# Performance work log

Measured on AMD Instinct MI355X. Metric: run time of the kernel, lower is better.

The kernel has to match this reference:

```python
import jax, jax.numpy as jnp
import numpy as np

N, S, W, H = 256, 64, 256, 32   # node_num, sensor_num, slide_win, gru_hid_size
ALPHA = 0.2
NEG = -9e15


def gat(h, adj, Wm, a):
    """pyGAT GraphAttentionLayer (concat=False, dropout=0 / eval).
    h: [..., M, din], adj: [..., M, M], Wm: [..., din, dout], a: [..., 2*dout]."""
    Wh = jnp.einsum('...mi,...io->...mo', h, Wm)
    dout = Wm.shape[-1]
    f1 = jnp.einsum('...mo,...o->...m', Wh, a[..., :dout])
    f2 = jnp.einsum('...mo,...o->...m', Wh, a[..., dout:])
    e = jax.nn.leaky_relu(f1[..., :, None] + f2[..., None, :], negative_slope=ALPHA)
    att = jax.nn.softmax(jnp.where(adj > 0, e, NEG), axis=-1)
    return jnp.einsum('...mk,...ko->...mo', att, Wh)


def gru_cell(h, x, Wih, Whh, bih, bhh):
    # per-node batched torch GRU cell; gate order r, z, n
    gi = jnp.einsum('ngi,ni->ng', Wih, x) + bih
    gh = jnp.einsum('ngh,nh->ng', Whh, h) + bhh
    ir, iz, inn = jnp.split(gi, 3, axis=-1)
    hr, hz, hn = jnp.split(gh, 3, axis=-1)
    r = jax.nn.sigmoid(ir + hr)
    z = jax.nn.sigmoid(iz + hz)
    n = jnp.tanh(inn + r * hn)
    return (1.0 - z) * n + z * h


def gru2(xseq, h0, Wih0, Whh0, bih0, bhh0, Wih1, Whh1, bih1, bhh1):
    # xseq: [N, S, Din] (seq axis = sensor axis), h0: [2, N, H] -> ([N,S,H], [2,N,H])
    def step(carry, x_t):
        h0c, h1c = carry
        h0n = gru_cell(h0c, x_t, Wih0, Whh0, bih0, bhh0)
        h1n = gru_cell(h1c, h0n, Wih1, Whh1, bih1, bhh1)
        return (h0n, h1n), h1n
    (h0f, h1f), ys = jax.lax.scan(step, (h0[0], h0[1]), jnp.swapaxes(xseq, 0, 1))
    return jnp.swapaxes(ys, 0, 1), jnp.stack([h0f, h1f])


def setup_inputs():
    key = jax.random.key(0)
    ks = jax.random.split(key, 32)
    def rn(k, shape, scale=0.05):
        return jax.random.normal(k, shape, dtype=jnp.float32) * scale
    inp = {}
    inp['x'] = jax.random.normal(ks[0], (N, S, W), dtype=jnp.float32)
    inp['Feature_adj_sub'] = jax.random.randint(ks[1], (N, S, S), 0, 2).astype(jnp.float32)
    inp['Time_adj_sub'] = jax.random.randint(ks[2], (N, W, W), 0, 2).astype(jnp.float32)
    inp['adj'] = jax.random.randint(ks[3], (N, N), 0, 2).astype(jnp.float32)
    inp['H_pre'] = jax.random.normal(ks[4], (2, N, H), dtype=jnp.float32)
    # per-node GAT params (stacked over nodes)
    inp['Fatt_W'] = rn(ks[5], (N, W, W)); inp['Fatt_a'] = rn(ks[6], (N, 2 * W))
    inp['Tatt_W'] = rn(ks[7], (N, S, S)); inp['Tatt_a'] = rn(ks[8], (N, 2 * S))
    # per-node 2-layer GRU params
    inp['Wih0'] = rn(ks[9], (N, 3 * H, 3 * W)); inp['Whh0'] = rn(ks[10], (N, 3 * H, H))
    inp['bih0'] = rn(ks[11], (N, 3 * H)); inp['bhh0'] = rn(ks[12], (N, 3 * H))
    inp['Wih1'] = rn(ks[13], (N, 3 * H, H)); inp['Whh1'] = rn(ks[14], (N, 3 * H, H))
    inp['bih1'] = rn(ks[15], (N, 3 * H)); inp['bhh1'] = rn(ks[16], (N, 3 * H))
    # per-node 3-layer FC
    inp['fc1_w'] = rn(ks[17], (N, H, H)); inp['fc1_b'] = rn(ks[18], (N, H))
    inp['fc2_w'] = rn(ks[19], (N, H, H)); inp['fc2_b'] = rn(ks[20], (N, H))
    inp['fc3_w'] = rn(ks[21], (N, 1, H)); inp['fc3_b'] = rn(ks[22], (N, 1))
    # global output GATs
    inp['oW'] = rn(ks[23], (S, S)); inp['oa'] = rn(ks[24], (2 * S,))
    inp['o1W'] = rn(ks[25], (S, S)); inp['o1a'] = rn(ks[26], (2 * S,))
    inp['o2W'] = rn(ks[27], (2 * S, S)); inp['o2a'] = rn(ks[28], (2 * S,))
    return inp


def reference(x, Feature_adj_sub, Time_adj_sub, adj, H_pre,
              Fatt_W, Fatt_a, Tatt_W, Tatt_a,
              Wih0, Whh0, bih0, bhh0, Wih1, Whh1, bih1, bhh1,
              fc1_w, fc1_b, fc2_w, fc2_b, fc3_w, fc3_b,
              oW, oa, o1W, o1a, o2W, o2a):
    # batched over all nodes at once (replaces Python loop over node_num)
    Fat = gat(x, Feature_adj_sub, Fatt_W, Fatt_a)                    # [N,S,W]
    Tat = gat(jnp.swapaxes(x, 1, 2), Time_adj_sub, Tatt_W, Tatt_a)   # [N,W,S]
    cat_at = jnp.concatenate([Fat, jnp.swapaxes(Tat, 1, 2), x], axis=-1)  # [N,S,3W]
    gru_out, cat_H = gru2(cat_at, H_pre, Wih0, Whh0, bih0, bhh0,
                          Wih1, Whh1, bih1, bhh1)                    # [N,S,H],[2,N,H]
    h = jax.nn.relu(jnp.einsum('nsh,nkh->nsk', gru_out, fc1_w) + fc1_b[:, None, :])
    h = jax.nn.relu(jnp.einsum('nsh,nkh->nsk', h, fc2_w) + fc2_b[:, None, :])
    ct = (jnp.einsum('nsh,nkh->nsk', h, fc3_w) + fc3_b[:, None, :])[..., 0]  # [N,S]
    out = gat(ct, adj, oW, oa)
    out1 = gat(ct, adj, o1W, o1a)
    finalout = gat(jnp.concatenate([out, out1], axis=-1), adj, o2W, o2a)
    return finalout, cat_H
```

## Files before the change

kernel.cpp:

```cpp
#include <hip/hip_runtime.h>
#include <hip/hip_bf16.h>

__device__ __forceinline__ float sigf(float x){ return __builtin_amdgcn_rcpf(1.f+__expf(-x)); }
__device__ __forceinline__ float tanhfa(float x){
  return 1.f - 2.f*__builtin_amdgcn_rcpf(1.f + __expf(2.f*x));
}

#define ALPHA 0.2f
#define NEGV  -9e15f


__device__ __forceinline__ void gl2lds16(const float* g, float* l){
  __builtin_amdgcn_global_load_lds(
      (const __attribute__((address_space(1))) void*)g,
      (__attribute__((address_space(3))) void*)l, 16, 0, 0);
}

__global__ __launch_bounds__(256) void k_mask(const float* __restrict__ src,
                                              unsigned* __restrict__ dst, int nelem){
  const int stride = gridDim.x * blockDim.x;
  const int lane = threadIdx.x & 63;
  for (int e = blockIdx.x*blockDim.x + threadIdx.x; e < nelem; e += stride){
    unsigned long long m = __ballot(src[e] > 0.f);
    if (lane == 0)       dst[e >> 5] = (unsigned)m;
    else if (lane == 32) dst[e >> 5] = (unsigned)(m >> 32);
  }
}

__global__ __launch_bounds__(256) void k3_wht(const float* __restrict__ x,
                                              const float* __restrict__ TW,
                                              const float* __restrict__ Ta,
                                              float* __restrict__ WhTt,
                                              float* __restrict__ Tf1p,
                                              float* __restrict__ Tf2p){
  const int n = blockIdx.x >> 1, ch = blockIdx.x & 1, c0 = ch*32;
  const int tid = threadIdx.x;
  __shared__ float Wm[64][36];
  __shared__ float as1[32], as2[32];
  for (int idx = tid; idx < 2048; idx += 256){
    int k = idx >> 5, cc = idx & 31;
    Wm[k][cc] = TW[n*4096 + k*64 + c0 + cc];
  }
  if (tid < 32){ as1[tid] = Ta[n*128 + c0 + tid]; as2[tid] = Ta[n*128 + 64 + c0 + tid]; }
  __syncthreads();
  const int i = tid;
  const float* xn = x + n*16384;
  float acc[32];
#pragma unroll
  for (int c = 0; c < 32; ++c) acc[c] = 0.f;
#pragma unroll 2
  for (int k = 0; k < 64; ++k){
    float xv = xn[k*256 + i];
    const float* wr = &Wm[k][0];
#pragma unroll
    for (int c = 0; c < 32; ++c) acc[c] = fmaf(xv, wr[c], acc[c]);
  }
  float f1 = 0.f, f2 = 0.f;
#pragma unroll
  for (int c = 0; c < 32; ++c){ f1 = fmaf(acc[c], as1[c], f1); f2 = fmaf(acc[c], as2[c], f2); }
  Tf1p[ch*65536 + n*256 + i] = f1;
  Tf2p[ch*65536 + n*256 + i] = f2;
  float* o = WhTt + n*16384 + i*64 + c0;
#pragma unroll
  for (int q = 0; q < 8; ++q)
    *(float4*)&o[4*q] = make_float4(acc[4*q], acc[4*q+1], acc[4*q+2], acc[4*q+3]);
}

__global__ __launch_bounds__(256) void k4_tat(const float* __restrict__ WhTt,
                                              const float* __restrict__ Tf1p,
                                              const float* __restrict__ Tf2p,
                                              const unsigned* __restrict__ maskT,
                                              float* __restrict__ TatT){
  const int n = blockIdx.x >> 1, ch = blockIdx.x & 1, c0 = ch*32;
  const int tid = threadIdx.x;
  __shared__ float wtL[8192];
  __shared__ float ptb[8192];
  __shared__ float f2s[256];
  __shared__ float ssum[256];
  __shared__ float wmax[4];
  {
    const int w = tid >> 6, l = tid & 63;
    const float* src = WhTt + n*16384 + (w*64 + (l>>3))*64 + c0 + (l&7)*4;
    float* dst = &wtL[w*2048];
#pragma unroll
    for (int r = 0; r < 8; ++r) gl2lds16(src + r*512, dst + r*256);
  }
  const float f1  = Tf1p[n*256 + tid] + Tf1p[65536 + n*256 + tid];
  const float f2v = Tf2p[n*256 + tid] + Tf2p[65536 + n*256 + tid];
  f2s[tid] = f2v;
  unsigned mw[8];
#pragma unroll
  for (int w = 0; w < 8; ++w) mw[w] = maskT[n*2048 + tid*8 + w];
  float wm = f2v;
#pragma unroll
  for (int d = 1; d < 64; d <<= 1) wm = fmaxf(wm, __shfl_xor(wm, d));
  if ((tid & 63) == 0) wmax[tid >> 6] = wm;
  asm volatile("s_waitcnt vmcnt(0)" ::: "memory");
  __syncthreads();
  const float mb = fmaxf(fmaxf(wmax[0], wmax[1]), fmaxf(wmax[2], wmax[3]));
  const float tm = f1 + mb;
  const float m  = (tm > 0.f) ? tm : ALPHA*tm;
  const int iq = tid & 63, cq = tid >> 6;
  float acc[4][8];
#pragma unroll
  for (int r = 0; r < 4; ++r)
#pragma unroll
    for (int c = 0; c < 8; ++c) acc[r][c] = 0.f;
  float sloc = 0.f;
  for (int jt = 0; jt < 8; ++jt){
    const int j0 = jt*32;
#pragma unroll
    for (int jj = 0; jj < 32; jj += 4){
      const float4 f2q = *(const float4*)&f2s[j0 + jj];
      const unsigned mk = mw[(j0 + jj) >> 5];
      const int sh = (j0 + jj) & 31;
      float t0 = f1 + f2q.x; t0 = (t0 > 0.f) ? t0 : ALPHA*t0;
      float t1 = f1 + f2q.y; t1 = (t1 > 0.f) ? t1 : ALPHA*t1;
      float t2 = f1 + f2q.z; t2 = (t2 > 0.f) ? t2 : ALPHA*t2;
      float t3 = f1 + f2q.w; t3 = (t3 > 0.f) ? t3 : ALPHA*t3;
      const float e0 = ((mk >> (sh+0)) & 1u) ? __expf(t0 - m) : 0.f;
      const float e1 = ((mk >> (sh+1)) & 1u) ? __expf(t1 - m) : 0.f;
      const float e2 = ((mk >> (sh+2)) & 1u) ? __expf(t2 - m) : 0.f;
      const float e3 = ((mk >> (sh+3)) & 1u) ? __expf(t3 - m) : 0.f;
      sloc += (e0 + e1) + (e2 + e3);
      ptb[(jj+0)*256 + tid] = e0;
      ptb[(jj+1)*256 + tid] = e1;
      ptb[(jj+2)*256 + tid] = e2;
      ptb[(jj+3)*256 + tid] = e3;
    }
    __syncthreads();
#pragma unroll 4
    for (int jj = 0; jj < 32; ++jj){
      const float4 p4 = *(const float4*)&ptb[jj*256 + 4*iq];
      const float4 w0 = *(const float4*)&wtL[(j0+jj)*32 + cq*8];
      const float4 w1 = *(const float4*)&wtL[(j0+jj)*32 + cq*8 + 4];
#pragma unroll
      for (int r = 0; r < 4; ++r){
        const float pv = (r == 0) ? p4.x : (r == 1) ? p4.y : (r == 2) ? p4.z : p4.w;
        acc[r][0] = fmaf(pv, w0.x, acc[r][0]);
        acc[r][1] = fmaf(pv, w0.y, acc[r][1]);
        acc[r][2] = fmaf(pv, w0.z, acc[r][2]);
        acc[r][3] = fmaf(pv, w0.w, acc[r][3]);
        acc[r][4] = fmaf(pv, w1.x, acc[r][4]);
        acc[r][5] = fmaf(pv, w1.y, acc[r][5]);
        acc[r][6] = fmaf(pv, w1.z, acc[r][6]);
        acc[r][7] = fmaf(pv, w1.w, acc[r][7]);
      }
    }
    __syncthreads();
  }
  ssum[tid] = sloc;
  __syncthreads();
  float* o = TatT + n*16384;
#pragma unroll
  for (int r = 0; r < 4; ++r){
    const int i2 = 4*iq + r;
    const float sv = ssum[i2];
    const float inv = (sv > 0.f) ? __builtin_amdgcn_rcpf(sv) : 0.f;
#pragma unroll
    for (int cc = 0; cc < 8; ++cc)
      o[(c0 + cq*8 + cc)*256 + i2] = acc[r][cc] * inv;
  }
}

__global__ __launch_bounds__(256) void k1_whf(const float* __restrict__ x,
                                              const float* __restrict__ FW,
                                              float* __restrict__ WhF){
  const int n = blockIdx.x >> 1, ch = blockIdx.x & 1, c0 = ch*128;
  const int tid = threadIdx.x;
  __shared__ float xt[16384];
  {
    const int w = tid >> 6, l = tid & 63;
    const float* xg = x + n*16384 + w*4096 + l*4;
    float* ld = &xt[w*4096];
#pragma unroll
    for (int j = 0; j < 16; ++j) gl2lds16(xg + j*256, ld + j*256);
  }
  asm volatile("s_waitcnt vmcnt(0)" ::: "memory");
  __syncthreads();
  const int cq = tid & 31, iq = tid >> 5;
  const int cc = c0 + cq*4;
  const float* Wn = FW + (size_t)n*65536 + cc;
  const float* xrow = &xt[iq*8*256];
  float acc[8][4];
#pragma unroll
  for (int i = 0; i < 8; ++i)
#pragma unroll
    for (int c = 0; c < 4; ++c) acc[i][c] = 0.f;
#pragma unroll 2
  for (int k4 = 0; k4 < 64; ++k4){
    const float4 w0 = *(const float4*)&Wn[(4*k4+0)*256];
    const float4 w1 = *(const float4*)&Wn[(4*k4+1)*256];
    const float4 w2 = *(const float4*)&Wn[(4*k4+2)*256];
    const float4 w3 = *(const float4*)&Wn[(4*k4+3)*256];
#pragma unroll
    for (int i = 0; i < 8; ++i){
      const float4 xv = *(const float4*)&xrow[i*256 + 4*k4];
      acc[i][0] = fmaf(xv.x, w0.x, acc[i][0]); acc[i][0] = fmaf(xv.y, w1.x, acc[i][0]);
      acc[i][0] = fmaf(xv.z, w2.x, acc[i][0]); acc[i][0] = fmaf(xv.w, w3.x, acc[i][0]);
      acc[i][1] = fmaf(xv.x, w0.y, acc[i][1]); acc[i][1] = fmaf(xv.y, w1.y, acc[i][1]);
      acc[i][1] = fmaf(xv.z, w2.y, acc[i][1]); acc[i][1] = fmaf(xv.w, w3.y, acc[i][1]);
      acc[i][2] = fmaf(xv.x, w0.z, acc[i][2]); acc[i][2] = fmaf(xv.y, w1.z, acc[i][2]);
      acc[i][2] = fmaf(xv.z, w2.z, acc[i][2]); acc[i][2] = fmaf(xv.w, w3.z, acc[i][2]);
      acc[i][3] = fmaf(xv.x, w0.w, acc[i][3]); acc[i][3] = fmaf(xv.y, w1.w, acc[i][3]);
      acc[i][3] = fmaf(xv.z, w2.w, acc[i][3]); acc[i][3] = fmaf(xv.w, w3.w, acc[i][3]);
    }
  }
  float* o = WhF + n*16384 + cc;
#pragma unroll
  for (int i = 0; i < 8; ++i)
    *(float4*)&o[(iq*8 + i)*256] = make_float4(acc[i][0], acc[i][1], acc[i][2], acc[i][3]);
}

__global__ __launch_bounds__(512) void k2_fat(const float* __restrict__ WhF,
                                              const float* __restrict__ Fa,
                                              const float* __restrict__ Fadj,
                                              float* __restrict__ Fat){
  const int n = blockIdx.x, tid = threadIdx.x;
  __shared__ float attT[64][68];
  __shared__ float f1s[64], f2s[64];
  __shared__ float part[64][8][2];
  const float* Wh = WhF + n*16384;
  {
    int i = tid >> 3, q = tid & 7;
    const float* an = Fa + n*512;
    float p1 = 0.f, p2 = 0.f;
    for (int cc = 0; cc < 32; ++cc){
      int c2 = q*32 + cc;
      float w = Wh[i*256 + c2];
      p1 = fmaf(w, an[c2], p1);
      p2 = fmaf(w, an[256 + c2], p2);
    }
    part[i][q][0] = p1; part[i][q][1] = p2;
  }
  __syncthreads();
  if (tid < 64){
    float s1 = 0.f, s2 = 0.f;
#pragma unroll
    for (int q = 0; q < 8; ++q){ s1 += part[tid][q][0]; s2 += part[tid][q][1]; }
    f1s[tid] = s1; f2s[tid] = s2;
  }
  __syncthreads();
  if (tid < 64){
    const int r = tid;
    const float f1 = f1s[r];
    const float* adjr = Fadj + n*4096 + r*64;
    unsigned m0 = 0, m1 = 0;
#pragma unroll
    for (int j = 0; j < 32; ++j) if (adjr[j] > 0.f) m0 |= (1u << j);
#pragma unroll
    for (int j = 0; j < 32; ++j) if (adjr[32+j] > 0.f) m1 |= (1u << j);
    float m = -INFINITY;
#pragma unroll
    for (int j = 0; j < 64; ++j){
      float e = f1 + f2s[j]; e = (e > 0.f) ? e : ALPHA*e;
      unsigned bit = (j < 32) ? ((m0 >> j) & 1u) : ((m1 >> (j-32)) & 1u);
      e = bit ? e : NEGV;
      m = fmaxf(m, e);
    }
    float s = 0.f;
#pragma unroll
    for (int j = 0; j < 64; ++j){
      float e = f1 + f2s[j]; e = (e > 0.f) ? e : ALPHA*e;
      unsigned bit = (j < 32) ? ((m0 >> j) & 1u) : ((m1 >> (j-32)) & 1u);
      e = bit ? e : NEGV;
      s += __expf(e - m);
    }
    const float inv = 1.f / s;
#pragma unroll
    for (int j = 0; j < 64; ++j){
      float e = f1 + f2s[j]; e = (e > 0.f) ? e : ALPHA*e;
      unsigned bit = (j < 32) ? ((m0 >> j) & 1u) : ((m1 >> (j-32)) & 1u);
      e = bit ? e : NEGV;
      attT[j][r] = __expf(e - m) * inv;
    }
  }
  __syncthreads();
  const int c = tid & 255, ih = tid >> 8;
  float acc[32];
#pragma unroll
  for (int i = 0; i < 32; ++i) acc[i] = 0.f;
#pragma unroll 2
  for (int j = 0; j < 64; ++j){
    float w = Wh[j*256 + c];
    const float* ar = &attT[j][ih*32];
#pragma unroll
    for (int i = 0; i < 32; ++i) acc[i] = fmaf(ar[i], w, acc[i]);
  }
  float* o = Fat + n*16384;
#pragma unroll
  for (int i = 0; i < 32; ++i) o[(ih*32 + i)*256 + c] = acc[i];
}

__global__ __launch_bounds__(256) void k5_gi0(const float* __restrict__ Fat,
                                              const float* __restrict__ TatT,
                                              const float* __restrict__ x,
                                              const float* __restrict__ Wih0,
                                              float* __restrict__ P0,
                                              float* __restrict__ P1,
                                              float* __restrict__ P2){
  const int n = blockIdx.x & 255, s = blockIdx.x >> 8;
  const int tid = threadIdx.x;
  const int l = tid & 63, w = tid >> 6;
  const int a = tid & 31, b = tid >> 5;
  __shared__ float cl[2][2048];
  __shared__ float wl[2][3072];
  const float* src = (s == 0) ? (Fat + n*16384)
                   : (s == 1) ? (TatT + n*16384)
                              : (x + n*16384);
  const float* Wseg = Wih0 + (size_t)n*73728 + s*256;
  const int lr = l >> 3, lc = l & 7, sc = lc ^ lr;
  const float* cg0 = src + (16*w + lr)*256 + sc*4;
  const float* cg1 = cg0 + 8*256;
  const float* wg0 = Wseg + (size_t)(24*w + lr)*768 + lc*4;
  const float* wg1 = wg0 + (size_t)8*768;
  const float* wg2 = wg0 + (size_t)16*768;

#define K5_STAGE(BF, K0) do {                       \
    gl2lds16(cg0 + (K0), &cl[BF][512*w]);           \
    gl2lds16(cg1 + (K0), &cl[BF][512*w + 256]);     \
    gl2lds16(wg0 + (K0), &wl[BF][768*w]);           \
    gl2lds16(wg1 + (K0), &wl[BF][768*w + 256]);     \
    gl2lds16(wg2 + (K0), &wl[BF][768*w + 512]);     \
  } while (0)

  float acc[12][2];
#pragma unroll
  for (int gi = 0; gi < 12; ++gi){ acc[gi][0] = 0.f; acc[gi][1] = 0.f; }

  int bf = 0;
  K5_STAGE(0, 0);
  const int ax4 = (a & 7) << 2;
#pragma unroll 1
  for (int kt = 0; kt < 8; ++kt){
    if (kt < 7){
      K5_STAGE(bf ^ 1, (kt + 1) * 32);
      asm volatile("s_waitcnt vmcnt(5)" ::: "memory");
    } else {
      asm volatile("s_waitcnt vmcnt(0)" ::: "memory");
    }
    __builtin_amdgcn_s_barrier();
    const float* clb  = &cl[bf][a*32];
    const float* clb2 = &cl[bf][(a+32)*32];
    const float* wlb  = &wl[bf][b*384];
#pragma unroll
    for (int k4 = 0; k4 < 8; ++k4){
      const int j4 = (k4 << 2) ^ ax4;
      const float4 c0 = *(const float4*)&clb[j4];
      const float4 c1 = *(const float4*)&clb2[j4];
#pragma unroll
      for (int gi = 0; gi < 12; ++gi){
        const float4 wv = *(const float4*)&wlb[gi*32 + (k4 << 2)];
        float a0 = acc[gi][0], a1 = acc[gi][1];
        a0 = fmaf(wv.x, c0.x, a0); a1 = fmaf(wv.x, c1.x, a1);
        a0 = fmaf(wv.y, c0.y, a0); a1 = fmaf(wv.y, c1.y, a1);
        a0 = fmaf(wv.z, c0.z, a0); a1 = fmaf(wv.z, c1.z, a1);
        a0 = fmaf(wv.w, c0.w, a0); a1 = fmaf(wv.w, c1.w, a1);
        acc[gi][0] = a0; acc[gi][1] = a1;
      }
    }
    __builtin_amdgcn_s_barrier();
    bf ^= 1;
  }
#undef K5_STAGE
  float* o = (s == 0) ? (P0 + n*16384)
           : (s == 1) ? (P1 + n*16384)
                      : (P2 + n*8192);
#pragma unroll
  for (int q = 0; q < 3; ++q){
    *(float4*)&o[a*96 + b*12 + q*4] =
        make_float4(acc[4*q][0], acc[4*q+1][0], acc[4*q+2][0], acc[4*q+3][0]);
    *(float4*)&o[(a+32)*96 + b*12 + q*4] =
        make_float4(acc[4*q][1], acc[4*q+1][1], acc[4*q+2][1], acc[4*q+3][1]);
  }
}

__global__ __launch_bounds__(128) void k6_gru(const float* __restrict__ G0,
                                              const float* __restrict__ G1,
                                              const float* __restrict__ G2,
                                              const float* __restrict__ Hpre,
                                              const float* __restrict__ Whh0,
                                              const float* __restrict__ bih0,
                                              const float* __restrict__ bhh0,
                                              const float* __restrict__ Wih1,
                                              const float* __restrict__ Whh1,
                                              const float* __restrict__ bih1,
                                              const float* __restrict__ bhh1,
                                              const float* __restrict__ fc1w,
                                              const float* __restrict__ fc1b,
                                              const float* __restrict__ fc2w,
                                              const float* __restrict__ fc2b,
                                              const float* __restrict__ fc3w,
                                              const float* __restrict__ fc3b,
                                              float* __restrict__ ct,
                                              float* __restrict__ dout){
  const int n = blockIdx.x, tid = threadIdx.x;
  const int wid = tid >> 6, l = tid & 63;
  const int g2 = l & 31, co = (l >> 5) * 16;
  __shared__ float ginS[6144];
  __shared__ float h0buf[2][32];
  __shared__ float h1buf[2][32];
  __shared__ float hist[64][33];
  __shared__ float Wst[32][33];
  __shared__ float b1s[32], b2s[32], w3s[32];
  {
    const float4* p0 = (const float4*)(G0 + n*16384);
    const float4* p1 = (const float4*)(G1 + n*16384);
    const float4* p2 = (const float4*)(G2 + n*8192);
    float4* gs = (float4*)ginS;
#pragma unroll
    for (int j = 0; j < 12; ++j){
      int idx = j*128 + tid;
      float4 a = p0[idx], b = p1[idx], c = p2[idx];
      gs[idx] = make_float4(a.x+b.x+c.x, a.y+b.y+c.y, a.z+b.z+c.z, a.w+b.w+c.w);
    }
  }
  if (tid < 32){
    b1s[tid] = fc1b[n*32 + tid];
    b2s[tid] = fc2b[n*32 + tid];
    w3s[tid] = fc3w[n*32 + tid];
  }
  for (int idx = tid; idx < 1024; idx += 128) Wst[idx>>5][idx&31] = fc1w[n*1024 + idx];
  float wr_[16], wz_[16], wn_[16];
  float ur_[16], uz_[16], un_[16];
  {
    const float* WA = (wid == 0) ? (Whh0 + n*3072) : (Wih1 + n*3072);
#pragma unroll
    for (int q = 0; q < 4; ++q){
      float4 v;
      v = *(const float4*)(WA + g2*32 + co + 4*q);       wr_[4*q]=v.x; wr_[4*q+1]=v.y; wr_[4*q+2]=v.z; wr_[4*q+3]=v.w;
      v = *(const float4*)(WA + (32+g2)*32 + co + 4*q);  wz_[4*q]=v.x; wz_[4*q+1]=v.y; wz_[4*q+2]=v.z; wz_[4*q+3]=v.w;
      v = *(const float4*)(WA + (64+g2)*32 + co + 4*q);  wn_[4*q]=v.x; wn_[4*q+1]=v.y; wn_[4*q+2]=v.z; wn_[4*q+3]=v.w;
    }
    if (wid == 1){
      const float* WB = Whh1 + n*3072;
#pragma unroll
      for (int q = 0; q < 4; ++q){
        float4 v;
        v = *(const float4*)(WB + g2*32 + co + 4*q);       ur_[4*q]=v.x; ur_[4*q+1]=v.y; ur_[4*q+2]=v.z; ur_[4*q+3]=v.w;
        v = *(const float4*)(WB + (32+g2)*32 + co + 4*q);  uz_[4*q]=v.x; uz_[4*q+1]=v.y; uz_[4*q+2]=v.z; uz_[4*q+3]=v.w;
        v = *(const float4*)(WB + (64+g2)*32 + co + 4*q);  un_[4*q]=v.x; un_[4*q+1]=v.y; un_[4*q+2]=v.z; un_[4*q+3]=v.w;
      }
    }
  }
  const float* bip = (wid == 0) ? bih0 : bih1;
  const float* bhp = (wid == 0) ? bhh0 : bhh1;
  const float br = bip[n*96 + g2], bz = bip[n*96 + 32 + g2], bn = bip[n*96 + 64 + g2];
  const float cr = bhp[n*96 + g2], cz = bhp[n*96 + 32 + g2], cn = bhp[n*96 + 64 + g2];
  const float* hp = (wid == 0) ? (Hpre + n*32) : (Hpre + 8192 + n*32);
  float hown = hp[g2];
  float hs[16];
#pragma unroll
  for (int q = 0; q < 4; ++q){
    float4 v = *(const float4*)&hp[co + 4*q];
    hs[4*q]=v.x; hs[4*q+1]=v.y; hs[4*q+2]=v.z; hs[4*q+3]=v.w;
  }
  for (int s = 0; s < 65; ++s){
    __syncthreads();
    if (wid == 0){
      if (s < 64){
        const float gr = ginS[s*96 + g2], gz = ginS[s*96 + 32 + g2], gn = ginS[s*96 + 64 + g2];
        if (s > 0){
#pragma unroll
          for (int q = 0; q < 4; ++q){
            float4 v = *(const float4*)&h0buf[(s-1)&1][co + 4*q];
            hs[4*q]=v.x; hs[4*q+1]=v.y; hs[4*q+2]=v.z; hs[4*q+3]=v.w;
          }
        }
        float pr = 0.f, pz = 0.f, pn = 0.f;
#pragma unroll
        for (int j = 0; j < 16; ++j){
          pr = fmaf(wr_[j], hs[j], pr);
          pz = fmaf(wz_[j], hs[j], pz);
          pn = fmaf(wn_[j], hs[j], pn);
        }
        pr += __shfl_xor(pr, 32);
        pz += __shfl_xor(pz, 32);
        pn += __shfl_xor(pn, 32);
        const float r = sigf(gr + br + pr + cr);
        const float z = sigf(gz + bz + pz + cz);
        const float nn = tanhfa(gn + bn + r*(pn + cn));
        hown = (1.f - z)*nn + z*hown;
        if (l < 32) h0buf[s & 1][g2] = hown;
      }
    } else {
      if (s >= 1){
        const int t = s - 1;
        if (s > 1){
#pragma unroll
          for (int q = 0; q < 4; ++q){
            float4 v = *(const float4*)&h1buf[(s-1)&1][co + 4*q];
            hs[4*q]=v.x; hs[4*q+1]=v.y; hs[4*q+2]=v.z; hs[4*q+3]=v.w;
          }
        }
        float hx[16];
#pragma unroll
        for (int q = 0; q < 4; ++q){
          float4 v = *(const float4*)&h0buf[(s-1)&1][co + 4*q];
          hx[4*q]=v.x; hx[4*q+1]=v.y; hx[4*q+2]=v.z; hx[4*q+3]=v.w;
        }
        float qr = 0.f, qz = 0.f, qn = 0.f, sr = 0.f, sz = 0.f, sn = 0.f;
#pragma unroll
        for (int j = 0; j < 16; ++j){
          qr = fmaf(wr_[j], hx[j], qr);  sr = fmaf(ur_[j], hs[j], sr);
          qz = fmaf(wz_[j], hx[j], qz);  sz = fmaf(uz_[j], hs[j], sz);
          qn = fmaf(wn_[j], hx[j], qn);  sn = fmaf(un_[j], hs[j], sn);
        }
        float vr = qr + sr; vr += __shfl_xor(vr, 32);
        float vz = qz + sz; vz += __shfl_xor(vz, 32);
        qn += __shfl_xor(qn, 32);
        sn += __shfl_xor(sn, 32);
        const float r1 = sigf(vr + br + cr);
        const float z1 = sigf(vz + bz + cz);
        const float n1 = tanhfa(qn + bn + r1*(sn + cn));
        hown = (1.f - z1)*n1 + z1*hown;
        if (l < 32){ h1buf[s & 1][g2] = hown; hist[t][g2] = hown; }
      }
    }
  }
  if (wid == 0 && l < 32) dout[16384 + n*32 + g2] = hown;
  if (wid == 1 && l < 32) dout[16384 + 8192 + n*32 + g2] = hown;
  __syncthreads();
  float r1a[32];
  if (tid < 64){
    float hr[32];
#pragma unroll
    for (int k = 0; k < 32; ++k) hr[k] = hist[tid][k];
#pragma unroll
    for (int k = 0; k < 32; ++k){
      float a0=0.f,a1=0.f,a2=0.f,a3=0.f;
#pragma unroll
      for (int q = 0; q < 32; q += 4){
        a0 = fmaf(hr[q],   Wst[k][q],   a0);
        a1 = fmaf(hr[q+1], Wst[k][q+1], a1);
        a2 = fmaf(hr[q+2], Wst[k][q+2], a2);
        a3 = fmaf(hr[q+3], Wst[k][q+3], a3);
      }
      float v = b1s[k] + ((a0+a1)+(a2+a3));
      r1a[k] = v > 0.f ? v : 0.f;
    }
  }
  __syncthreads();
  for (int idx = tid; idx < 1024; idx += 128) Wst[idx>>5][idx&31] = fc2w[n*1024 + idx];
  __syncthreads();
  if (tid < 64){
    float r2a[32];
#pragma unroll
    for (int k = 0; k < 32; ++k){
      float a0=0.f,a1=0.f,a2=0.f,a3=0.f;
#pragma unroll
      for (int q = 0; q < 32; q += 4){
        a0 = fmaf(r1a[q],   Wst[k][q],   a0);
        a1 = fmaf(r1a[q+1], Wst[k][q+1], a1);
        a2 = fmaf(r1a[q+2], Wst[k][q+2], a2);
        a3 = fmaf(r1a[q+3], Wst[k][q+3], a3);
      }
      float v = b2s[k] + ((a0+a1)+(a2+a3));
      r2a[k] = v > 0.f ? v : 0.f;
    }
    float v = fc3b[n];
#pragma unroll
    for (int k = 0; k < 32; ++k) v = fmaf(r2a[k], w3s[k], v);
    ct[n*64 + tid] = v;
  }
}

__global__ __launch_bounds__(256) void k8a(const float* __restrict__ ct,
                                           const float* __restrict__ W0,
                                           const float* __restrict__ a0,
                                           const float* __restrict__ W1,
                                           const float* __restrict__ a1,
                                           float* __restrict__ WhABt,
                                           float* __restrict__ OF1,
                                           float* __restrict__ OF2){
  const int gat = blockIdx.x >> 2, rq = blockIdx.x & 3, r0 = rq*64;
  const int tid = threadIdx.x;
  const int ii = tid & 63, cq = tid >> 6;
  __shared__ float ctl[64][65];
  __shared__ float Wl[64][68];
  __shared__ float a1s[64], a2s[64];
  __shared__ float red[64][4][2];
  const float* W = gat ? W1 : W0;
  const float* aa = gat ? a1 : a0;
  for (int idx = tid; idx < 4096; idx += 256){
    int i2 = idx >> 6, k = idx & 63;
    ctl[i2][k] = ct[(r0 + i2)*64 + k];
  }
  for (int idx = tid; idx < 4096; idx += 256){
    int k = idx >> 6, c = idx & 63;
    Wl[k][c] = W[k*64 + c];
  }
  if (tid < 64){ a1s[tid] = aa[tid]; a2s[tid] = aa[64 + tid]; }
  __syncthreads();
  float acc[16];
#pragma unroll
  for (int c = 0; c < 16; ++c) acc[c] = 0.f;
#pragma unroll 2
  for (int k = 0; k < 64; ++k){
    float v = ctl[ii][k];
    const float* wr = &Wl[k][cq*16];
#pragma unroll
    for (int c = 0; c < 16; ++c) acc[c] = fmaf(v, wr[c], acc[c]);
  }
  float p1 = 0.f, p2 = 0.f;
#pragma unroll
  for (int c = 0; c < 16; ++c){
    p1 = fmaf(acc[c], a1s[cq*16 + c], p1);
    p2 = fmaf(acc[c], a2s[cq*16 + c], p2);
  }
  red[ii][cq][0] = p1; red[ii][cq][1] = p2;
  float* o = WhABt + gat*16384;
#pragma unroll
  for (int c = 0; c < 16; ++c) o[(cq*16 + c)*256 + r0 + ii] = acc[c];
  __syncthreads();
  if (cq == 0){
    OF1[gat*256 + r0 + ii] = red[ii][0][0] + red[ii][1][0] + red[ii][2][0] + red[ii][3][0];
    OF2[gat*256 + r0 + ii] = red[ii][0][1] + red[ii][1][1] + red[ii][2][1] + red[ii][3][1];
  }
}

__global__ __launch_bounds__(256) void k8b(const float* __restrict__ WhABt,
                                           const float* __restrict__ OF1,
                                           const float* __restrict__ OF2,
                                           const unsigned* __restrict__ maskA,
                                           float* __restrict__ OUTT){
  const int gat = blockIdx.x >> 2, c0 = (blockIdx.x & 3) * 16;
  const int i = threadIdx.x;
  __shared__ float wt[4096];
  __shared__ float f2s[256];
  __shared__ float wmax[4];
  {
    const int w = i >> 6, l = i & 63;
    const float* src = WhABt + gat*16384 + c0*256 + w*1024 + l*4;
    float* dst = &wt[w*1024];
#pragma unroll
    for (int r = 0; r < 4; ++r) gl2lds16(src + r*256, dst + r*256);
  }
  const float f1  = OF1[gat*256 + i];
  const float f2v = OF2[gat*256 + i];
  f2s[i] = f2v;
  unsigned mw[8];
#pragma unroll
  for (int w = 0; w < 8; ++w) mw[w] = maskA[i*8 + w];
  float wm = f2v;
#pragma unroll
  for (int d = 1; d < 64; d <<= 1) wm = fmaxf(wm, __shfl_xor(wm, d));
  if ((i & 63) == 0) wmax[i >> 6] = wm;
  asm volatile("s_waitcnt vmcnt(0)" ::: "memory");
  __syncthreads();
  const float mb = fmaxf(fmaxf(wmax[0], wmax[1]), fmaxf(wmax[2], wmax[3]));
  const float tm = f1 + mb;
  const float m  = (tm > 0.f) ? tm : ALPHA*tm;
  float acc[16];
#pragma unroll
  for (int c = 0; c < 16; ++c) acc[c] = 0.f;
  float s = 0.f;
#pragma unroll 2
  for (int jb = 0; jb < 64; ++jb){
    const float4 f2q = *(const float4*)&f2s[jb*4];
    const unsigned mk = mw[jb >> 3];
    const int sh = (jb & 7) * 4;
    float t0 = f1 + f2q.x; t0 = (t0 > 0.f) ? t0 : ALPHA*t0;
    float t1 = f1 + f2q.y; t1 = (t1 > 0.f) ? t1 : ALPHA*t1;
    float t2 = f1 + f2q.z; t2 = (t2 > 0.f) ? t2 : ALPHA*t2;
    float t3 = f1 + f2q.w; t3 = (t3 > 0.f) ? t3 : ALPHA*t3;
    const float e0 = ((mk >> (sh+0)) & 1u) ? __expf(t0 - m) : 0.f;
    const float e1 = ((mk >> (sh+1)) & 1u) ? __expf(t1 - m) : 0.f;
    const float e2 = ((mk >> (sh+2)) & 1u) ? __expf(t2 - m) : 0.f;
    const float e3 = ((mk >> (sh+3)) & 1u) ? __expf(t3 - m) : 0.f;
    s += (e0 + e1) + (e2 + e3);
#pragma unroll
    for (int c = 0; c < 16; ++c){
      const float4 wv = *(const float4*)&wt[c*256 + jb*4];
      acc[c] = fmaf(e0, wv.x, fmaf(e1, wv.y, fmaf(e2, wv.z, fmaf(e3, wv.w, acc[c]))));
    }
  }
  const float inv = (s > 0.f) ? __builtin_amdgcn_rcpf(s) : 0.f;
#pragma unroll
  for (int c = 0; c < 16; ++c) OUTT[gat*16384 + (c0+c)*256 + i] = acc[c] * inv;
}

__global__ __launch_bounds__(256) void k8c(const float* __restrict__ OUTT,
                                           const float* __restrict__ W2,
                                           const float* __restrict__ a2,
                                           float* __restrict__ Wh2,
                                           float* __restrict__ F1B,
                                           float* __restrict__ F2B){
  const int r0 = blockIdx.x * 32;
  const int tid = threadIdx.x;
  const int ii = tid & 31, cq = tid >> 5;
  __shared__ float W2l[128][68];
  __shared__ float a1s[64], a2s[64];
  __shared__ float red[32][8][2];
  for (int idx = tid; idx < 8192; idx += 256){
    int k = idx >> 6, c = idx & 63;
    W2l[k][c] = W2[k*64 + c];
  }
  if (tid < 64){ a1s[tid] = a2[tid]; a2s[tid] = a2[64 + tid]; }
  __syncthreads();
  float acc[8];
#pragma unroll
  for (int c = 0; c < 8; ++c) acc[c] = 0.f;
#pragma unroll 2
  for (int k = 0; k < 128; ++k){
    float v = OUTT[(k >> 6)*16384 + (k & 63)*256 + r0 + ii];
    const float* wr = &W2l[k][cq*8];
#pragma unroll
    for (int c = 0; c < 8; ++c) acc[c] = fmaf(v, wr[c], acc[c]);
  }
  float p1 = 0.f, p2 = 0.f;
#pragma unroll
  for (int c = 0; c < 8; ++c){
    p1 = fmaf(acc[c], a1s[cq*8 + c], p1);
    p2 = fmaf(acc[c], a2s[cq*8 + c], p2);
  }
  red[ii][cq][0] = p1; red[ii][cq][1] = p2;
#pragma unroll
  for (int c = 0; c < 8; ++c) Wh2[(cq*8 + c)*256 + r0 + ii] = acc[c];
  __syncthreads();
  if (cq == 0){
    float s1 = 0.f, s2 = 0.f;
#pragma unroll
    for (int q = 0; q < 8; ++q){ s1 += red[ii][q][0]; s2 += red[ii][q][1]; }
    F1B[r0 + ii] = s1; F2B[r0 + ii] = s2;
  }
}

__global__ __launch_bounds__(256) void k8d(const float* __restrict__ Wh2,
                                           const float* __restrict__ F1B,
                                           const float* __restrict__ F2B,
                                           const unsigned* __restrict__ maskA,
                                           float* __restrict__ dOut){
  const int c0 = blockIdx.x * 16;
  const int i = threadIdx.x;
  __shared__ float wt[4096];
  __shared__ float f2s[256];
  __shared__ float wmax[4];
  {
    const int w = i >> 6, l = i & 63;
    const float* src = Wh2 + c0*256 + w*1024 + l*4;
    float* dst = &wt[w*1024];
#pragma unroll
    for (int r = 0; r < 4; ++r) gl2lds16(src + r*256, dst + r*256);
  }
  const float f1  = F1B[i];
  const float f2v = F2B[i];
  f2s[i] = f2v;
  unsigned mw[8];
#pragma unroll
  for (int w = 0; w < 8; ++w) mw[w] = maskA[i*8 + w];
  float wm = f2v;
#pragma unroll
  for (int d = 1; d < 64; d <<= 1) wm = fmaxf(wm, __shfl_xor(wm, d));
  if ((i & 63) == 0) wmax[i >> 6] = wm;
  asm volatile("s_waitcnt vmcnt(0)" ::: "memory");
  __syncthreads();
  const float mb = fmaxf(fmaxf(wmax[0], wmax[1]), fmaxf(wmax[2], wmax[3]));
  const float tm = f1 + mb;
  const float m  = (tm > 0.f) ? tm : ALPHA*tm;
  float acc[16];
#pragma unroll
  for (int c = 0; c < 16; ++c) acc[c] = 0.f;
  float s = 0.f;
#pragma unroll 2
  for (int jb = 0; jb < 64; ++jb){
    const float4 f2q = *(const float4*)&f2s[jb*4];
    const unsigned mk = mw[jb >> 3];
    const int sh = (jb & 7) * 4;
    float t0 = f1 + f2q.x; t0 = (t0 > 0.f) ? t0 : ALPHA*t0;
    float t1 = f1 + f2q.y; t1 = (t1 > 0.f) ? t1 : ALPHA*t1;
    float t2 = f1 + f2q.z; t2 = (t2 > 0.f) ? t2 : ALPHA*t2;
    float t3 = f1 + f2q.w; t3 = (t3 > 0.f) ? t3 : ALPHA*t3;
    const float e0 = ((mk >> (sh+0)) & 1u) ? __expf(t0 - m) : 0.f;
    const float e1 = ((mk >> (sh+1)) & 1u) ? __expf(t1 - m) : 0.f;
    const float e2 = ((mk >> (sh+2)) & 1u) ? __expf(t2 - m) : 0.f;
    const float e3 = ((mk >> (sh+3)) & 1u) ? __expf(t3 - m) : 0.f;
    s += (e0 + e1) + (e2 + e3);
#pragma unroll
    for (int c = 0; c < 16; ++c){
      const float4 wv = *(const float4*)&wt[c*256 + jb*4];
      acc[c] = fmaf(e0, wv.x, fmaf(e1, wv.y, fmaf(e2, wv.z, fmaf(e3, wv.w, acc[c]))));
    }
  }
  const float inv = (s > 0.f) ? __builtin_amdgcn_rcpf(s) : 0.f;
#pragma unroll
  for (int c = 0; c < 16; ++c) dOut[i*64 + c0 + c] = acc[c] * inv;
}

extern "C" void kernel_launch(void* const* d_in, const int* in_sizes, int n_in,
                              void* d_out, int out_size, void* d_ws, size_t ws_size,
                              hipStream_t stream){
  (void)in_sizes; (void)n_in; (void)out_size; (void)ws_size;
  const float* x     = (const float*)d_in[0];
  const float* Fadj  = (const float*)d_in[1];
  const float* Tadj  = (const float*)d_in[2];
  const float* adj   = (const float*)d_in[3];
  const float* Hpre  = (const float*)d_in[4];
  const float* FattW = (const float*)d_in[5];
  const float* Fatta = (const float*)d_in[6];
  const float* TattW = (const float*)d_in[7];
  const float* Tatta = (const float*)d_in[8];
  const float* Wih0  = (const float*)d_in[9];
  const float* Whh0  = (const float*)d_in[10];
  const float* bih0  = (const float*)d_in[11];
  const float* bhh0  = (const float*)d_in[12];
  const float* Wih1  = (const float*)d_in[13];
  const float* Whh1  = (const float*)d_in[14];
  const float* bih1  = (const float*)d_in[15];
  const float* bhh1  = (const float*)d_in[16];
  const float* fc1w  = (const float*)d_in[17];
  const float* fc1b  = (const float*)d_in[18];
  const float* fc2w  = (const float*)d_in[19];
  const float* fc2b  = (const float*)d_in[20];
  const float* fc3w  = (const float*)d_in[21];
  const float* fc3b  = (const float*)d_in[22];
  const float* oW    = (const float*)d_in[23];
  const float* oa    = (const float*)d_in[24];
  const float* o1W   = (const float*)d_in[25];
  const float* o1a   = (const float*)d_in[26];
  const float* o2W   = (const float*)d_in[27];
  const float* o2a   = (const float*)d_in[28];
  float* out = (float*)d_out;

  float* ws = (float*)d_ws;
  float* R0 = ws;
  float* R1 = ws + 4194304;
  float* R2 = ws + 8388608;
  unsigned* maskT = (unsigned*)R2;
  float* Tf1p = R2 + 524288;
  float* Tf2p = R2 + 655360;
  unsigned* maskA = (unsigned*)(ws + 12582912);
  float* WhTt = R0;
  float* WhF  = R0;
  float* TatT = R1;
  float* Fat  = R2;
  float* P0 = R2;
  float* P1 = R1;
  float* P2 = R0;
  float* ctb   = R0 + 2097152;
  float* WhABt = R1 + 16384;
  float* OF1   = R1 + 49152;
  float* OF2   = R1 + 49664;
  float* OUTT  = R1 + 50176;
  float* WH2   = R1 + 82944;
  float* F1B   = R1 + 99328;
  float* F2B   = R1 + 99584;

  k_mask<<<1024, 256, 0, stream>>>(Tadj, maskT, 16777216);
  k_mask<<<32, 256, 0, stream>>>(adj, maskA, 65536);
  k3_wht<<<512, 256, 0, stream>>>(x, TattW, Tatta, WhTt, Tf1p, Tf2p);
  k4_tat<<<512, 256, 0, stream>>>(WhTt, Tf1p, Tf2p, maskT, TatT);
  k1_whf<<<512, 256, 0, stream>>>(x, FattW, WhF);
  k2_fat<<<256, 512, 0, stream>>>(WhF, Fatta, Fadj, Fat);
  k5_gi0<<<768, 256, 0, stream>>>(Fat, TatT, x, Wih0, P0, P1, P2);
  k6_gru<<<256, 128, 0, stream>>>(P0, P1, P2, Hpre, Whh0, bih0, bhh0, Wih1, Whh1, bih1, bhh1,
                                  fc1w, fc1b, fc2w, fc2b, fc3w, fc3b, ctb, out);
  k8a<<<8, 256, 0, stream>>>(ctb, oW, oa, o1W, o1a, WhABt, OF1, OF2);
  k8b<<<8, 256, 0, stream>>>(WhABt, OF1, OF2, maskA, OUTT);
  k8c<<<8, 256, 0, stream>>>(OUTT, o2W, o2a, WH2, F1B, F2B);
  k8d<<<4, 256, 0, stream>>>(WH2, F1B, F2B, maskA, out);
}
```

Measured before the change: 605.2 us.

## Read GRU input weights directly from global memory; stage activations via registers

```diff
diff --git a/kernel.cpp b/kernel.cpp
--- a/kernel.cpp
+++ b/kernel.cpp
@@ -301,68 +301,60 @@
                                               float* __restrict__ P2){
   const int n = blockIdx.x & 255, s = blockIdx.x >> 8;
   const int tid = threadIdx.x;
-  const int l = tid & 63, w = tid >> 6;
   const int a = tid & 31, b = tid >> 5;
-  __shared__ float cl[2][2048];
-  __shared__ float wl[2][3072];
+  __shared__ float cl[2][2304];
   const float* src = (s == 0) ? (Fat + n*16384)
                    : (s == 1) ? (TatT + n*16384)
                               : (x + n*16384);
-  const float* Wseg = Wih0 + (size_t)n*73728 + s*256;
-  const int lr = l >> 3, lc = l & 7, sc = lc ^ lr;
-  const float* cg0 = src + (16*w + lr)*256 + sc*4;
-  const float* cg1 = cg0 + 8*256;
-  const float* wg0 = Wseg + (size_t)(24*w + lr)*768 + lc*4;
-  const float* wg1 = wg0 + (size_t)8*768;
-  const float* wg2 = wg0 + (size_t)16*768;
-
-#define K5_STAGE(BF, K0) do {                       \
-    gl2lds16(cg0 + (K0), &cl[BF][512*w]);           \
-    gl2lds16(cg1 + (K0), &cl[BF][512*w + 256]);     \
-    gl2lds16(wg0 + (K0), &wl[BF][768*w]);           \
-    gl2lds16(wg1 + (K0), &wl[BF][768*w + 256]);     \
-    gl2lds16(wg2 + (K0), &wl[BF][768*w + 512]);     \
-  } while (0)
-
+  const float* Wseg = Wih0 + (size_t)n*73728 + s*256 + (size_t)b*12*768;
+  const int tr = tid >> 2, kq = tid & 3;
+  const float* cg = src + tr*256 + kq*8;
+  const int cwo = tr*36 + kq*8;
+  {
+    float4 ra = *(const float4*)cg;
+    float4 rb = *(const float4*)(cg + 4);
+    *(float4*)&cl[0][cwo]     = ra;
+    *(float4*)&cl[0][cwo + 4] = rb;
+  }
+  __syncthreads();
   float acc[12][2];
 #pragma unroll
   for (int gi = 0; gi < 12; ++gi){ acc[gi][0] = 0.f; acc[gi][1] = 0.f; }
-
-  int bf = 0;
-  K5_STAGE(0, 0);
-  const int ax4 = (a & 7) << 2;
 #pragma unroll 1
   for (int kt = 0; kt < 8; ++kt){
+    const int buf = kt & 1;
+    float4 na, nb;
     if (kt < 7){
-      K5_STAGE(bf ^ 1, (kt + 1) * 32);
-      asm volatile("s_waitcnt vmcnt(5)" ::: "memory");
-    } else {
-      asm volatile("s_waitcnt vmcnt(0)" ::: "memory");
-    }
-    __builtin_amdgcn_s_barrier();
-    const float* clb  = &cl[bf][a*32];
-    const float* clb2 = &cl[bf][(a+32)*32];
-    const float* wlb  = &wl[bf][b*384];
+      na = *(const float4*)(cg + (kt+1)*32);
+      nb = *(const float4*)(cg + (kt+1)*32 + 4);
+    }
+    const float* Wk = Wseg + kt*32;
+    const float* c0p = &cl[buf][a*36];
+    const float* c1p = &cl[buf][(a+32)*36];
 #pragma unroll
     for (int k4 = 0; k4 < 8; ++k4){
-      const int j4 = (k4 << 2) ^ ax4;
-      const float4 c0 = *(const float4*)&clb[j4];
-      const float4 c1 = *(const float4*)&clb2[j4];
+      float4 wv[12];
+#pragma unroll
+      for (int gi = 0; gi < 12; ++gi)
+        wv[gi] = *(const float4*)(Wk + (size_t)gi*768 + k4*4);
+      const float4 c0 = *(const float4*)(c0p + k4*4);
+      const float4 c1 = *(const float4*)(c1p + k4*4);
 #pragma unroll
       for (int gi = 0; gi < 12; ++gi){
-        const float4 wv = *(const float4*)&wlb[gi*32 + (k4 << 2)];
         float a0 = acc[gi][0], a1 = acc[gi][1];
-        a0 = fmaf(wv.x, c0.x, a0); a1 = fmaf(wv.x, c1.x, a1);
-        a0 = fmaf(wv.y, c0.y, a0); a1 = fmaf(wv.y, c1.y, a1);
-        a0 = fmaf(wv.z, c0.z, a0); a1 = fmaf(wv.z, c1.z, a1);
-        a0 = fmaf(wv.w, c0.w, a0); a1 = fmaf(wv.w, c1.w, a1);
+        a0 = fmaf(wv[gi].x, c0.x, a0); a1 = fmaf(wv[gi].x, c1.x, a1);
+        a0 = fmaf(wv[gi].y, c0.y, a0); a1 = fmaf(wv[gi].y, c1.y, a1);
+        a0 = fmaf(wv[gi].z, c0.z, a0); a1 = fmaf(wv[gi].z, c1.z, a1);
+        a0 = fmaf(wv[gi].w, c0.w, a0); a1 = fmaf(wv[gi].w, c1.w, a1);
         acc[gi][0] = a0; acc[gi][1] = a1;
       }
     }
-    __builtin_amdgcn_s_barrier();
-    bf ^= 1;
-  }
-#undef K5_STAGE
+    if (kt < 7){
+      *(float4*)&cl[buf^1][cwo]     = na;
+      *(float4*)&cl[buf^1][cwo + 4] = nb;
+    }
+    __syncthreads();
+  }
   float* o = (s == 0) ? (P0 + n*16384)
            : (s == 1) ? (P1 + n*16384)
                       : (P2 + n*8192);
```

New measurement: 655.7 us. 1.08x slower.

## Retile GRU input-projection kernel to 4 rows per thread with split-K reduction

Applied to the files above, without the earlier changes.

```diff
diff --git a/kernel.cpp b/kernel.cpp
--- a/kernel.cpp
+++ b/kernel.cpp
@@ -302,16 +302,20 @@
   const int n = blockIdx.x & 255, s = blockIdx.x >> 8;
   const int tid = threadIdx.x;
   const int l = tid & 63, w = tid >> 6;
-  const int a = tid & 31, b = tid >> 5;
+  const int b = tid >> 5;
+  const int kg = (tid >> 4) & 1;
+  const int ta = tid & 15;
   __shared__ float cl[2][2048];
   __shared__ float wl[2][3072];
   const float* src = (s == 0) ? (Fat + n*16384)
                    : (s == 1) ? (TatT + n*16384)
                               : (x + n*16384);
   const float* Wseg = Wih0 + (size_t)n*73728 + s*256;
-  const int lr = l >> 3, lc = l & 7, sc = lc ^ lr;
-  const float* cg0 = src + (16*w + lr)*256 + sc*4;
-  const float* cg1 = cg0 + 8*256;
+  const int lr = l >> 3, lc = l & 7;
+  const int sc0 = lc ^ ((4*w + (lr >> 2)) & 7);
+  const int sc1 = lc ^ ((4*w + 2 + (lr >> 2)) & 7);
+  const float* cg0 = src + (16*w + lr)*256 + sc0*4;
+  const float* cg1 = src + (16*w + 8 + lr)*256 + sc1*4;
   const float* wg0 = Wseg + (size_t)(24*w + lr)*768 + lc*4;
   const float* wg1 = wg0 + (size_t)8*768;
   const float* wg2 = wg0 + (size_t)16*768;
@@ -324,13 +328,15 @@
     gl2lds16(wg2 + (K0), &wl[BF][768*w + 512]);     \
   } while (0)
 
-  float acc[12][2];
-#pragma unroll
-  for (int gi = 0; gi < 12; ++gi){ acc[gi][0] = 0.f; acc[gi][1] = 0.f; }
+  float acc[12][4];
+#pragma unroll
+  for (int gi = 0; gi < 12; ++gi)
+#pragma unroll
+    for (int r = 0; r < 4; ++r) acc[gi][r] = 0.f;
 
   int bf = 0;
   K5_STAGE(0, 0);
-  const int ax4 = (a & 7) << 2;
+  const int t7 = ta & 7;
 #pragma unroll 1
   for (int kt = 0; kt < 8; ++kt){
     if (kt < 7){
@@ -340,38 +346,60 @@
       asm volatile("s_waitcnt vmcnt(0)" ::: "memory");
     }
     __builtin_amdgcn_s_barrier();
-    const float* clb  = &cl[bf][a*32];
-    const float* clb2 = &cl[bf][(a+32)*32];
-    const float* wlb  = &wl[bf][b*384];
-#pragma unroll
-    for (int k4 = 0; k4 < 8; ++k4){
-      const int j4 = (k4 << 2) ^ ax4;
-      const float4 c0 = *(const float4*)&clb[j4];
-      const float4 c1 = *(const float4*)&clb2[j4];
+    const float* wb = &wl[bf][b*384 + kg*16];
+    const float* cb = &cl[bf][ta*128];
+#pragma unroll
+    for (int k4 = 0; k4 < 4; ++k4){
+      const int q4 = (((kg*4 + k4) ^ t7)) * 4;
+      const float4 c0 = *(const float4*)&cb[0*32 + q4];
+      const float4 c1 = *(const float4*)&cb[1*32 + q4];
+      const float4 c2 = *(const float4*)&cb[2*32 + q4];
+      const float4 c3 = *(const float4*)&cb[3*32 + q4];
 #pragma unroll
       for (int gi = 0; gi < 12; ++gi){
-        const float4 wv = *(const float4*)&wlb[gi*32 + (k4 << 2)];
-        float a0 = acc[gi][0], a1 = acc[gi][1];
+        const float4 wv = *(const float4*)&wb[gi*32 + k4*4];
+        float a0 = acc[gi][0], a1 = acc[gi][1], a2 = acc[gi][2], a3 = acc[gi][3];
         a0 = fmaf(wv.x, c0.x, a0); a1 = fmaf(wv.x, c1.x, a1);
+        a2 = fmaf(wv.x, c2.x, a2); a3 = fmaf(wv.x, c3.x, a3);
         a0 = fmaf(wv.y, c0.y, a0); a1 = fmaf(wv.y, c1.y, a1);
+        a2 = fmaf(wv.y, c2.y, a2); a3 = fmaf(wv.y, c3.y, a3);
         a0 = fmaf(wv.z, c0.z, a0); a1 = fmaf(wv.z, c1.z, a1);
+        a2 = fmaf(wv.z, c2.z, a2); a3 = fmaf(wv.z, c3.z, a3);
         a0 = fmaf(wv.w, c0.w, a0); a1 = fmaf(wv.w, c1.w, a1);
-        acc[gi][0] = a0; acc[gi][1] = a1;
+        a2 = fmaf(wv.w, c2.w, a2); a3 = fmaf(wv.w, c3.w, a3);
+        acc[gi][0] = a0; acc[gi][1] = a1; acc[gi][2] = a2; acc[gi][3] = a3;
       }
     }
     __builtin_amdgcn_s_barrier();
     bf ^= 1;
   }
 #undef K5_STAGE
-  float* o = (s == 0) ? (P0 + n*16384)
-           : (s == 1) ? (P1 + n*16384)
-                      : (P2 + n*8192);
-#pragma unroll
-  for (int q = 0; q < 3; ++q){
-    *(float4*)&o[a*96 + b*12 + q*4] =
-        make_float4(acc[4*q][0], acc[4*q+1][0], acc[4*q+2][0], acc[4*q+3][0]);
-    *(float4*)&o[(a+32)*96 + b*12 + q*4] =
-        make_float4(acc[4*q][1], acc[4*q+1][1], acc[4*q+2][1], acc[4*q+3][1]);
+  const int idx128 = b*16 + ta;
+  float* red = &wl[0][0];
+  if (kg == 1){
+#pragma unroll
+    for (int gi = 0; gi < 12; ++gi)
+      *(float4*)&red[idx128*48 + gi*4] =
+          make_float4(acc[gi][0], acc[gi][1], acc[gi][2], acc[gi][3]);
+  }
+  __syncthreads();
+  if (kg == 0){
+#pragma unroll
+    for (int gi = 0; gi < 12; ++gi){
+      const float4 v = *(const float4*)&red[idx128*48 + gi*4];
+      acc[gi][0] += v.x; acc[gi][1] += v.y; acc[gi][2] += v.z; acc[gi][3] += v.w;
+    }
+    float* o = (s == 0) ? (P0 + n*16384)
+             : (s == 1) ? (P1 + n*16384)
+                        : (P2 + n*8192);
+#pragma unroll
+    for (int r = 0; r < 4; ++r){
+      const int t = ta*4 + r;
+#pragma unroll
+      for (int qq = 0; qq < 3; ++qq)
+        *(float4*)&o[t*96 + b*12 + qq*4] =
+            make_float4(acc[4*qq][r], acc[4*qq+1][r], acc[4*qq+2][r], acc[4*qq+3][r]);
+    }
   }
 }
 
```

Result: faster. 585.4 us (-3.3%).
